# Performance work log

Measured on AMD Instinct MI355X. Metric: run time of the kernel, lower is better.

Reference implementation:

```python
import jax, jax.numpy as jnp
import numpy as np

BBOX_STD = np.array([0.1, 0.1, 0.2, 0.2], np.float32)
MIN_CONF = 0.7
MAX_INST = 100
NMS_THR = 0.3


def setup_inputs() -> dict:
    key = jax.random.key(0)
    k1, k2, k3 = jax.random.split(key, 3)
    B, N, C = 8, 1000, 81
    # rois: valid normalized boxes (y1<=y2, x1<=x2)
    pts = jax.random.uniform(k1, (B, N, 2, 2), dtype=jnp.float32)
    lo = jnp.min(pts, axis=2)   # [B,N,2] -> (y1,x1)
    hi = jnp.max(pts, axis=2)   # [B,N,2] -> (y2,x2)
    rois = jnp.concatenate([lo, hi], axis=-1)
    # confident softmax class probabilities
    logits = 5.0 * jax.random.normal(k2, (B, N, C), dtype=jnp.float32)
    mrcnn_class = jax.nn.softmax(logits, axis=-1)
    mrcnn_bbox = 0.2 * jax.random.normal(k3, (B, N, C, 4), dtype=jnp.float32)
    # image_meta: [id(1), orig_shape(3), image_shape(3), window(4), scale(1), active_class_ids(81)]
    meta = np.zeros((B, 1 + 3 + 3 + 4 + 1 + C), np.float32)
    meta[:, 1:4] = [1024.0, 1024.0, 3.0]
    meta[:, 4:7] = [1024.0, 1024.0, 3.0]
    meta[:, 7:11] = [0.0, 0.0, 1024.0, 1024.0]
    meta[:, 11] = 1.0
    return {"rois": rois, "mrcnn_class": mrcnn_class,
            "mrcnn_bbox": mrcnn_bbox, "image_meta": jnp.asarray(meta)}


def _apply_box_deltas(boxes, deltas):
    # boxes/deltas: [N,4] (y1,x1,y2,x2) / (dy,dx,log dh,log dw)
    h = boxes[:, 2] - boxes[:, 0]
    w = boxes[:, 3] - boxes[:, 1]
    cy = boxes[:, 0] + 0.5 * h
    cx = boxes[:, 1] + 0.5 * w
    cy = cy + deltas[:, 0] * h
    cx = cx + deltas[:, 1] * w
    h = h * jnp.exp(deltas[:, 2])
    w = w * jnp.exp(deltas[:, 3])
    return jnp.stack([cy - 0.5 * h, cx - 0.5 * w, cy + 0.5 * h, cx + 0.5 * w], axis=1)


def _clip_boxes(boxes, window):
    wy1, wx1, wy2, wx2 = window[0], window[1], window[2], window[3]
    y1 = jnp.clip(boxes[:, 0], wy1, wy2)
    x1 = jnp.clip(boxes[:, 1], wx1, wx2)
    y2 = jnp.clip(boxes[:, 2], wy1, wy2)
    x2 = jnp.clip(boxes[:, 3], wx1, wx2)
    return jnp.stack([y1, x1, y2, x2], axis=1)


def _iou_matrix(boxes):
    # boxes: [N,4] -> pairwise IoU [N,N]
    y1, x1, y2, x2 = boxes[:, 0], boxes[:, 1], boxes[:, 2], boxes[:, 3]
    area = (y2 - y1) * (x2 - x1)
    iy1 = jnp.maximum(y1[:, None], y1[None, :])
    ix1 = jnp.maximum(x1[:, None], x1[None, :])
    iy2 = jnp.minimum(y2[:, None], y2[None, :])
    ix2 = jnp.minimum(x2[:, None], x2[None, :])
    inter = jnp.maximum(iy2 - iy1, 0.0) * jnp.maximum(ix2 - ix1, 0.0)
    union = area[:, None] + area[None, :] - inter
    return inter / jnp.maximum(union, 1e-10)


def _refine_one_image(rois, probs, deltas, window):
    N = rois.shape[0]
    idx = jnp.arange(N)
    class_ids = jnp.argmax(probs, axis=1)                 # [N]
    class_scores = probs[idx, class_ids]                  # [N]
    deltas_spec = deltas[idx, class_ids] * jnp.asarray(BBOX_STD)
    refined = _clip_boxes(_apply_box_deltas(rois, deltas_spec), window)
    # filter: background and low-confidence
    valid = (class_ids > 0) & (class_scores >= MIN_CONF)
    scores = jnp.where(valid, class_scores, -1.0)
    # sort by score desc, greedy class-aware NMS (== per-class NMS merged)
    order = jnp.argsort(-scores)
    boxes_s = refined[order]
    scores_s = scores[order]
    cls_s = class_ids[order]
    iou = _iou_matrix(boxes_s)                            # [N,N]
    suppress = (iou > NMS_THR) & (cls_s[:, None] == cls_s[None, :])
    keep0 = scores_s > -0.5

    def body(i, keep):
        sup = suppress[i] & keep[i] & (jnp.arange(N) > i)
        return keep & (~sup)

    keep = jax.lax.fori_loop(0, N, body, keep0)
    final_scores = jnp.where(keep, scores_s, -1.0)
    top_scores, top_idx = jax.lax.top_k(final_scores, MAX_INST)
    ok = top_scores > -0.5                                # [MAX_INST]
    out_boxes = jnp.where(ok[:, None], boxes_s[top_idx], 0.0)
    out_cls = jnp.where(ok, cls_s[top_idx].astype(jnp.float32), 0.0)
    out_scr = jnp.where(ok, top_scores, 0.0)
    return jnp.concatenate([out_boxes, out_cls[:, None], out_scr[:, None]], axis=1)


def reference(rois, mrcnn_class, mrcnn_bbox, image_meta):
    # parse image meta: image_shape = meta[:,4:7], window (pixels) = meta[:,7:11]
    image_shape = image_meta[0, 4:7]
    h, w = image_shape[0], image_shape[1]
    scale = jnp.stack([h, w, h, w]) - 1.0
    shift = jnp.array([0.0, 0.0, 1.0, 1.0], jnp.float32)
    window = (image_meta[:, 7:11] - shift) / scale        # [B,4] normalized
    dets = jax.vmap(_refine_one_image)(rois, mrcnn_class, mrcnn_bbox, window)
    return dets  # [B, MAX_INST, 6]
```

## Files before the change

### kernel.cpp

```cpp
#include <hip/hip_runtime.h>


#define NROI 1000
#define NCLS 81
#define MAXI 100
#define PAD  1024
#define BLK  1024
#define NW   (BLK / 64)
#define MIN_CONF 0.7f
#define NMS_THR  0.3f

typedef float f32x4u __attribute__((ext_vector_type(4), aligned(4)));
typedef unsigned long long u64;

__device__ __forceinline__ u64 shfl_xor_u64(u64 v, int m) {
  unsigned lo = (unsigned)__shfl_xor((int)(unsigned)(v & 0xFFFFFFFFull), m, 64);
  unsigned hi = (unsigned)__shfl_xor((int)(unsigned)(v >> 32), m, 64);
  return (((u64)hi) << 32) | lo;
}

__global__ __launch_bounds__(64) void refine_kernel(
    const float* __restrict__ rois,
    const float* __restrict__ probs,
    const float* __restrict__ deltas,
    const float* __restrict__ meta,
    float4* __restrict__ ws_box,
    float2* __restrict__ ws_aux,
    int meta_stride)
{
  const int b   = blockIdx.x >> 4;
  const int roi = ((blockIdx.x & 15) << 6) + threadIdx.x;
  if (roi >= NROI) return;

  const float* p = probs + ((size_t)b * NROI + roi) * NCLS;
  float best = p[0];
  int   bc = 0;
  for (int c0 = 1; c0 < NCLS; c0 += 4) {
    f32x4u v = *(const f32x4u*)(p + c0);
#pragma unroll
    for (int e = 0; e < 4; ++e) {
      float f = v[e];
      if (f > best) { best = f; bc = c0 + e; }
    }
  }

  const float4 dd = *(const float4*)(deltas + (((size_t)b * NROI + roi) * NCLS + bc) * 4);
  const float4 rr = *(const float4*)(rois + ((size_t)b * NROI + roi) * 4);

  float hh = rr.z - rr.x, ww = rr.w - rr.y;
  float cy = rr.x + 0.5f * hh + (dd.x * 0.1f) * hh;
  float cx = rr.y + 0.5f * ww + (dd.y * 0.1f) * ww;
  hh *= expf(dd.z * 0.2f);
  ww *= expf(dd.w * 0.2f);
  float ny1 = cy - 0.5f * hh, nx1 = cx - 0.5f * ww;
  float ny2 = cy + 0.5f * hh, nx2 = cx + 0.5f * ww;

  float H = meta[4], W = meta[5];
  float sy = H - 1.0f, sx = W - 1.0f;
  const float* m = meta + (size_t)b * meta_stride;
  float wy1 = m[7] / sy, wx1 = m[8] / sx;
  float wy2 = (m[9] - 1.0f) / sy, wx2 = (m[10] - 1.0f) / sx;

  float4 bb;
  bb.x = fminf(fmaxf(ny1, wy1), wy2);
  bb.y = fminf(fmaxf(nx1, wx1), wx2);
  bb.z = fminf(fmaxf(ny2, wy1), wy2);
  bb.w = fminf(fmaxf(nx2, wx1), wx2);

  bool valid = (bc > 0) && (best >= MIN_CONF);
  float score = valid ? best : -1.0f;

  ws_box[(size_t)b * PAD + roi] = bb;
  ws_aux[(size_t)b * PAD + roi] = make_float2(score, (float)bc);
}

__global__ __launch_bounds__(BLK) void sortnms_kernel(
    const float4* __restrict__ ws_box,
    const float2* __restrict__ ws_aux,
    float* __restrict__ out)
{
  const int b    = blockIdx.x;
  const int tid  = threadIdx.x;
  const int lane = tid & 63;
  const int wv   = tid >> 6;

  __shared__ u64    skey[BLK];
  __shared__ float4 sbox[NROI];
  __shared__ float  ssc[NROI];
  __shared__ int    scls[NROI];
  __shared__ u64    cmask[NCLS];
  __shared__ u64    s_alive;
  __shared__ int    wcnt[NW];

  for (int k = tid; k < MAXI * 6; k += BLK)
    out[(size_t)b * (MAXI * 6) + k] = 0.0f;

  float sc = (tid < NROI) ? ws_aux[(size_t)b * PAD + tid].x : -1.0f;
  const bool valid = sc > -0.5f;
  skey[tid] = 0xFFFFFFFFFFFFFFFFull;

  u64 vb = __ballot(valid);
  if (lane == 0) wcnt[wv] = (int)__popcll(vb);
  __syncthreads();
  int V = 0, cbase0 = 0;
  for (int w = 0; w < NW; ++w) {
    int c = wcnt[w];
    if (w < wv) cbase0 += c;
    V += c;
  }
  if (valid) {
    int slot = cbase0 + (int)__popcll(vb & ((1ull << (unsigned)lane) - 1ull));
    unsigned bits = __float_as_uint(sc);
    unsigned ord  = (bits & 0x80000000u) ? ~bits : (bits | 0x80000000u);
    skey[slot] = (((u64)(~ord)) << 32) | (unsigned)tid;
  }
  __syncthreads();

  int P = 64;
  while (P < V) P <<= 1;
  const bool insort = tid < P;

  u64 key = skey[tid];
  for (int k = 2; k <= P; k <<= 1) {
    for (int j = k >> 1; j > 0; j >>= 1) {
      const bool takeMin = (((tid & j) == 0) == ((tid & k) == 0));
      if (j >= 64) {
        if (insort) skey[tid] = key;
        __syncthreads();
        if (insort) {
          u64 other = skey[tid ^ j];
          const bool take = takeMin ? (other < key) : (other > key);
          key = take ? other : key;
        }
        __syncthreads();
      } else if (insort) {
        u64 other = shfl_xor_u64(key, j);
        const bool take = takeMin ? (other < key) : (other > key);
        key = take ? other : key;
      }
    }
  }

  if (tid < V) {
    int orig = (int)(key & 0xFFFFFFFFull);
    float2 a = ws_aux[(size_t)b * PAD + orig];
    sbox[tid] = ws_box[(size_t)b * PAD + orig];
    ssc[tid]  = a.x;
    scls[tid] = (int)a.y;
  }
  __syncthreads();

  bool   mykeep = tid < V;
  float4 jb = make_float4(0.f, 0.f, 0.f, 0.f);
  float  jarea = 0.f;
  int    jcls = -1;
  if (mykeep) {
    jb = sbox[tid];
    jcls = scls[tid];
    jarea = (jb.z - jb.x) * (jb.w - jb.y);
  }

  int kc = 0;
  const int nchunks = (V + 63) >> 6;
  for (int c = 0; c < nchunks; ++c) {
    if (tid < NCLS) cmask[tid] = 0ull;
    __syncthreads();
    if (wv == c && mykeep) atomicOr(&cmask[jcls], 1ull << (unsigned)lane);
    __syncthreads();

    u64 jsup = 0ull;
    if (mykeep && wv >= c) {
      u64 m = cmask[jcls];
      if (wv == c) m &= (1ull << (unsigned)lane) - 1ull;
      const int cb = c << 6;
      while (m) {
        int l = __ffsll((long long)m) - 1;
        m &= m - 1;
        float4 lb = sbox[cb + l];
        float la = (lb.z - lb.x) * (lb.w - lb.y);
        float iy1 = fmaxf(lb.x, jb.x), ix1 = fmaxf(lb.y, jb.y);
        float iy2 = fminf(lb.z, jb.z), ix2 = fminf(lb.w, jb.w);
        float inter = fmaxf(iy2 - iy1, 0.f) * fmaxf(ix2 - ix1, 0.f);
        if (inter > NMS_THR * fmaxf(la + jarea - inter, 1e-10f))
          jsup |= (1ull << (unsigned)l);
      }
    }

    if (wv == c) {
      u64 aliveW = __ballot(mykeep);
      u64 rem = aliveW;
      while (rem) {
        int l = __ffsll((long long)rem) - 1;
        rem &= ~(1ull << (unsigned)l);
        u64 kill = __ballot((int)((jsup >> (unsigned)l) & 1ull));
        aliveW &= ~kill;
        rem    &= ~kill;
      }
      mykeep = ((aliveW >> (unsigned)lane) & 1ull) != 0;
      if (lane == 0) s_alive = aliveW;
    }
    __syncthreads();
    const u64 alive = s_alive;
    if (wv > c && (jsup & alive)) mykeep = false;
    kc += (int)__popcll(alive);
    if (kc >= MAXI) break;
  }

  u64 bm = __ballot((int)mykeep);
  if (lane == 0) wcnt[wv] = (int)__popcll(bm);
  __syncthreads();
  if (mykeep) {
    int base2 = 0;
    for (int q = 0; q < wv; ++q) base2 += wcnt[q];
    int slot = base2 + (int)__popcll(bm & ((1ull << (unsigned)lane) - 1ull));
    if (slot < MAXI) {
      float* o = out + ((size_t)b * MAXI + slot) * 6;
      o[0] = jb.x; o[1] = jb.y; o[2] = jb.z; o[3] = jb.w;
      o[4] = (float)jcls;
      o[5] = ssc[tid];
    }
  }
}

extern "C" void kernel_launch(void* const* d_in, const int* in_sizes, int n_in,
                              void* d_out, int out_size, void* d_ws, size_t ws_size,
                              hipStream_t stream) {
  const float* rois   = (const float*)d_in[0];
  const float* probs  = (const float*)d_in[1];
  const float* deltas = (const float*)d_in[2];
  const float* meta   = (const float*)d_in[3];
  float* out = (float*)d_out;

  const int nb = in_sizes[0] / (NROI * 4);
  const int meta_stride = in_sizes[3] / nb;

  float4* ws_box = (float4*)d_ws;
  float2* ws_aux = (float2*)((char*)d_ws + (size_t)nb * PAD * sizeof(float4));

  refine_kernel<<<nb * 16, 64, 0, stream>>>(rois, probs, deltas, meta,
                                            ws_box, ws_aux, meta_stride);
  sortnms_kernel<<<nb, BLK, 0, stream>>>(ws_box, ws_aux, out);
}
```

Baseline: 26.43 us.

## Pack class into sort key, double-buffer bitonic stages, precompute per-chunk class masks

The sort key now holds the original index and class id, and the score is recovered from the key bits. This removes the post-sort gather of aux data from global memory. The cross-wave bitonic steps alternate between two shared buffers, so each step needs one barrier instead of two. Per-wave class masks are built once before NMS rather than rebuilt with two barriers per chunk, at the cost of more shared memory and the assumption that scores are non-negative.

```diff
diff --git a/kernel.cpp b/kernel.cpp
--- a/kernel.cpp
+++ b/kernel.cpp
@@ -84,20 +84,25 @@
   const int lane = tid & 63;
   const int wv   = tid >> 6;
 
-  __shared__ u64    skey[BLK];
+  __shared__ u64    skeyA[BLK], skeyB[BLK];
+  __shared__ float4 u_box[NROI];
   __shared__ float4 sbox[NROI];
-  __shared__ float  ssc[NROI];
-  __shared__ int    scls[NROI];
-  __shared__ u64    cmask[NCLS];
-  __shared__ u64    s_alive;
+  __shared__ u64    cmask[NW][NCLS];
+  __shared__ u64    s_alive[NW];
   __shared__ int    wcnt[NW];
 
   for (int k = tid; k < MAXI * 6; k += BLK)
     out[(size_t)b * (MAXI * 6) + k] = 0.0f;
 
-  float sc = (tid < NROI) ? ws_aux[(size_t)b * PAD + tid].x : -1.0f;
+  float sc = -1.0f;
+  int   cls = 0;
+  if (tid < NROI) {
+    float2 a = ws_aux[(size_t)b * PAD + tid];
+    sc  = a.x;
+    cls = (int)a.y;
+    u_box[tid] = ws_box[(size_t)b * PAD + tid];
+  }
   const bool valid = sc > -0.5f;
-  skey[tid] = 0xFFFFFFFFFFFFFFFFull;
 
   u64 vb = __ballot(valid);
   if (lane == 0) wcnt[wv] = (int)__popcll(vb);
@@ -111,8 +116,13 @@
   if (valid) {
     int slot = cbase0 + (int)__popcll(vb & ((1ull << (unsigned)lane) - 1ull));
     unsigned bits = __float_as_uint(sc);
-    unsigned ord  = (bits & 0x80000000u) ? ~bits : (bits | 0x80000000u);
-    skey[slot] = (((u64)(~ord)) << 32) | (unsigned)tid;
+    unsigned ord  = bits | 0x80000000u;
+    skeyA[slot] = (((u64)(~ord)) << 32) | ((unsigned)tid << 7) | (unsigned)cls;
+  }
+  if (tid >= V) skeyA[tid] = 0xFFFFFFFFFFFFFFFFull;
+  {
+    u64* cf = &cmask[0][0];
+    for (int i = tid; i < NW * NCLS; i += BLK) cf[i] = 0ull;
   }
   __syncthreads();
 
@@ -120,59 +130,50 @@
   while (P < V) P <<= 1;
   const bool insort = tid < P;
 
-  u64 key = skey[tid];
+  u64 key = skeyA[tid];
+  int ldst = 1;
   for (int k = 2; k <= P; k <<= 1) {
     for (int j = k >> 1; j > 0; j >>= 1) {
       const bool takeMin = (((tid & j) == 0) == ((tid & k) == 0));
       if (j >= 64) {
-        if (insort) skey[tid] = key;
+        u64* buf = (ldst & 1) ? skeyB : skeyA;
+        if (insort) buf[tid] = key;
         __syncthreads();
         if (insort) {
-          u64 other = skey[tid ^ j];
-          const bool take = takeMin ? (other < key) : (other > key);
-          key = take ? other : key;
+          u64 other = buf[tid ^ j];
+          key = (takeMin ? (other < key) : (other > key)) ? other : key;
         }
-        __syncthreads();
+        ++ldst;
       } else if (insort) {
         u64 other = shfl_xor_u64(key, j);
-        const bool take = takeMin ? (other < key) : (other > key);
-        key = take ? other : key;
+        key = (takeMin ? (other < key) : (other > key)) ? other : key;
       }
     }
   }
-
-  if (tid < V) {
-    int orig = (int)(key & 0xFFFFFFFFull);
-    float2 a = ws_aux[(size_t)b * PAD + orig];
-    sbox[tid] = ws_box[(size_t)b * PAD + orig];
-    ssc[tid]  = a.x;
-    scls[tid] = (int)a.y;
-  }
-  __syncthreads();
 
   bool   mykeep = tid < V;
   float4 jb = make_float4(0.f, 0.f, 0.f, 0.f);
   float  jarea = 0.f;
   int    jcls = -1;
   if (mykeep) {
-    jb = sbox[tid];
-    jcls = scls[tid];
+    int oid = (int)((key >> 7) & 0x3FFull);
+    jcls = (int)(key & 0x7Full);
+    jb = u_box[oid];
     jarea = (jb.z - jb.x) * (jb.w - jb.y);
-  }
+    sbox[tid] = jb;
+    atomicOr(&cmask[wv][jcls], 1ull << (unsigned)lane);
+  }
+  __syncthreads();
 
   int kc = 0;
   const int nchunks = (V + 63) >> 6;
   for (int c = 0; c < nchunks; ++c) {
-    if (tid < NCLS) cmask[tid] = 0ull;
-    __syncthreads();
-    if (wv == c && mykeep) atomicOr(&cmask[jcls], 1ull << (unsigned)lane);
-    __syncthreads();
+    const int cb = c << 6;
 
     u64 jsup = 0ull;
     if (mykeep && wv >= c) {
-      u64 m = cmask[jcls];
+      u64 m = cmask[c][jcls];
       if (wv == c) m &= (1ull << (unsigned)lane) - 1ull;
-      const int cb = c << 6;
       while (m) {
         int l = __ffsll((long long)m) - 1;
         m &= m - 1;
@@ -197,10 +198,10 @@
         rem    &= ~kill;
       }
       mykeep = ((aliveW >> (unsigned)lane) & 1ull) != 0;
-      if (lane == 0) s_alive = aliveW;
+      if (lane == 0) s_alive[c] = aliveW;
     }
     __syncthreads();
-    const u64 alive = s_alive;
+    const u64 alive = s_alive[c];
     if (wv > c && (jsup & alive)) mykeep = false;
     kc += (int)__popcll(alive);
     if (kc >= MAXI) break;
@@ -214,10 +215,12 @@
     for (int q = 0; q < wv; ++q) base2 += wcnt[q];
     int slot = base2 + (int)__popcll(bm & ((1ull << (unsigned)lane) - 1ull));
     if (slot < MAXI) {
+      unsigned ordhi = ~(unsigned)(key >> 32);
+      float score = __uint_as_float(ordhi & 0x7FFFFFFFu);
       float* o = out + ((size_t)b * MAXI + slot) * 6;
       o[0] = jb.x; o[1] = jb.y; o[2] = jb.z; o[3] = jb.w;
       o[4] = (float)jcls;
-      o[5] = ssc[tid];
+      o[5] = score;
     }
   }
 }
```

Result: slower. 27.07 us (+2.4%).
